# Kernel tuning notes

Measured on AMD Instinct MI355X. Metric: run time of the kernel, lower is better.

## Reference

```python
import jax, jax.numpy as jnp
import numpy as np
import math

K = 7
B, C, H, W = 16, 3, 256, 256
N = 50000
ANGLE = 30.0; TRANS = 0.45; SHEAR = 0.3; SCALE0, SCALE1 = 1.0, 0.5  # self.scale assumed [1.0,0.5] (upstream AutoDO)


def _bilinear(img, xs, ys):
    # img: (C,Hs,Ws); xs,ys: (Ho,Wo) pixel coords; border padding (clamp)
    Cc, Hs, Ws = img.shape
    xs = jnp.clip(xs, 0.0, Ws - 1.0)
    ys = jnp.clip(ys, 0.0, Hs - 1.0)
    x0 = jnp.floor(xs); y0 = jnp.floor(ys)
    wx = xs - x0; wy = ys - y0
    x0i = x0.astype(jnp.int32); y0i = y0.astype(jnp.int32)
    x1i = jnp.minimum(x0i + 1, Ws - 1); y1i = jnp.minimum(y0i + 1, Hs - 1)
    Ia = img[:, y0i, x0i]; Ib = img[:, y0i, x1i]
    Ic = img[:, y1i, x0i]; Id = img[:, y1i, x1i]
    return Ia * (1 - wx) * (1 - wy) + Ib * wx * (1 - wy) + Ic * (1 - wx) * wy + Id * wx * wy


def _resize(x, Ho, Wo):
    # torch F.interpolate bilinear, align_corners=False, no antialias
    Bb, Cc, Hs, Ws = x.shape
    ys = (jnp.arange(Ho, dtype=x.dtype) + 0.5) * (Hs / Ho) - 0.5
    xs = (jnp.arange(Wo, dtype=x.dtype) + 0.5) * (Ws / Wo) - 0.5
    Y, X = jnp.meshgrid(ys, xs, indexing='ij')
    return jax.vmap(lambda im: _bilinear(im, X, Y))(x)


def _warp_perspective(x, M, Ho, Wo):
    # kornia.warp_perspective: dst(p) = src(M^-1 p), bilinear, border padding, align_corners=True
    Bb, Cc, Hs, Ws = x.shape
    Minv = jnp.linalg.inv(M)  # (B,3,3)
    yy, xx = jnp.meshgrid(jnp.arange(Ho, dtype=x.dtype), jnp.arange(Wo, dtype=x.dtype), indexing='ij')
    pts = jnp.stack([xx.ravel(), yy.ravel(), jnp.ones(Ho * Wo, dtype=x.dtype)])  # (3, Ho*Wo)
    src = jnp.einsum('bij,jn->bin', Minv, pts)
    xs = (src[:, 0] / src[:, 2]).reshape(Bb, Ho, Wo)
    ys = (src[:, 1] / src[:, 2]).reshape(Bb, Ho, Wo)
    return jax.vmap(_bilinear)(x, xs, ys)


def _forward(x, paramP, paramM, gumbel_u, eps, idx):
    dt = x.dtype
    pP = jax.nn.sigmoid(paramP[:, idx])  # (K,B)
    logits = jnp.stack([jnp.log(pP).ravel(), jnp.log(1.0 - pP).ravel()], axis=1)  # (K*B,2)
    g = -jnp.log(-jnp.log(gumbel_u))
    y_soft = jax.nn.softmax(logits + g, axis=1)  # tau=1
    y_hard = jax.nn.one_hot(jnp.argmax(y_soft, axis=1), 2, dtype=y_soft.dtype)
    y = y_hard + y_soft - jax.lax.stop_gradient(y_soft)  # straight-through hard gumbel
    sP = y[:, 0].reshape(K, B)
    sM = jax.nn.sigmoid(paramM[:, idx]) * eps  # (K,B)
    ang = sP[0] * sM[0] * ANGLE
    # replicate torch's cat(W//2 * ones(B), H//2 * ones(B)).view(-1,2) layout exactly
    ctr = jnp.concatenate([jnp.full((B,), W // 2, dt), jnp.full((B,), H // 2, dt)]).reshape(-1, 2)
    sx = SCALE0 + sP[5] * sM[5] * SCALE1
    sy = SCALE0 + sP[6] * sM[6] * SCALE1
    rad = jnp.deg2rad(ang); ca = jnp.cos(rad); sa = jnp.sin(rad)
    # kornia get_rotation_matrix2d: rot=[[c,s],[-s,c]] @ diag(sx,sy); t = ctr - rot@ctr
    sr = jnp.stack([jnp.stack([ca * sx, sa * sy], -1), jnp.stack([-sa * sx, ca * sy], -1)], -2)  # (B,2,2)
    t = ctr - jnp.einsum('bij,bj->bi', sr, ctr)
    eye = jnp.broadcast_to(jnp.eye(3, dtype=dt), (B, 3, 3))
    R = eye.at[:, :2, :2].set(sr).at[:, :2, 2].set(t)
    T = eye.at[:, 0, 2].set(W * sP[1] * sM[1] * TRANS).at[:, 1, 2].set(H * sP[2] * sM[2] * TRANS)
    S = eye.at[:, 0, 1].set(sP[3] * sM[3] * SHEAR).at[:, 1, 0].set(sP[4] * sM[4] * SHEAR)
    M = S @ T @ R
    x_up = _resize(x, 4 * H, 4 * W)
    x_w = _warp_perspective(x_up, M, 4 * H, 4 * W)
    return _resize(x_w, H, W)


def setup_inputs() -> dict:
    key = jax.random.key(0)
    k1, k2, k3, k4 = jax.random.split(key, 4)
    p = 1.0 / (K - 2)
    prob_logit = math.log(p / (1.0 - p))
    m = 5.0 / 10.0
    magn_logit = math.log(m / (1.0 - m))
    return {
        'x': jax.random.uniform(k1, (B, C, H, W), jnp.float32),
        'paramP': jnp.full((K, N), prob_logit, jnp.float32),
        'paramM': jnp.full((K, N), magn_logit, jnp.float32),
        'gumbel_u': jax.random.uniform(k2, (K * B, 2), jnp.float32, minval=1e-6, maxval=1.0 - 1e-6),
        'eps': jax.random.normal(k3, (K, B), jnp.float32),
        'idx': jax.random.randint(k4, (B,), 0, N, jnp.int32),
    }


def reference(x, paramP, paramM, gumbel_u, eps, idx):
    return _forward(x, paramP, paramM, gumbel_u, eps, idx)
```

## Files before the change

### kernel.cpp

```cpp
#include <hip/hip_runtime.h>
#include <math.h>


typedef float floatx4 __attribute__((ext_vector_type(4)));

__device__ __forceinline__ floatx4 load4(const float* p) {
    floatx4 v;
    __builtin_memcpy(&v, p, sizeof(v));
    return v;
}

struct Up { int i0; float w; };

__device__ __forceinline__ Up upc(int v) {
    float u = fmaf(0.25f, (float)v, -0.375f);
    u = fminf(fmaxf(u, 0.0f), 255.0f);
    float f = floorf(u);
    Up r; r.i0 = (int)f; r.w = u - f;
    return r;
}

struct Trip { float w0, w1, w2; int base; };

__device__ __forceinline__ Trip merged3(float s) {
    float f = floorf(s);
    float fr = s - f;
    int v0 = (int)f;
    int v1 = min(v0 + 1, 1023);
    Up c0 = upc(v0), c1 = upc(v1);
    float A0 = 1.0f - fr, A1 = fr;
    float b0 = A1 * (1.0f - c1.w), b1 = A1 * c1.w;
    bool d = (c1.i0 != c0.i0);
    Trip t;
    t.w0 = A0 * (1.0f - c0.w) + (d ? 0.0f : b0);
    t.w1 = A0 * c0.w + (d ? b0 : b1);
    t.w2 = d ? b1 : 0.0f;
    t.base = c0.i0;
    return t;
}

__device__ __forceinline__ void pair_accum(
    Trip cA, Trip cB, Trip rA, Trip rB,
    const float* __restrict__ xb, float* acc)
{
    int cb = min(cA.base, cB.base);
    int rb = min(rA.base, rB.base);
    float CA[4], CB[4], RA[4], RB[4];
    bool sa_ = (cA.base != cb);
    CA[0] = sa_ ? 0.f : cA.w0;  CA[1] = sa_ ? cA.w0 : cA.w1;
    CA[2] = sa_ ? cA.w1 : cA.w2;  CA[3] = sa_ ? cA.w2 : 0.f;
    bool sb_ = (cB.base != cb);
    CB[0] = sb_ ? 0.f : cB.w0;  CB[1] = sb_ ? cB.w0 : cB.w1;
    CB[2] = sb_ ? cB.w1 : cB.w2;  CB[3] = sb_ ? cB.w2 : 0.f;
    bool ra_ = (rA.base != rb);
    RA[0] = ra_ ? 0.f : rA.w0;  RA[1] = ra_ ? rA.w0 : rA.w1;
    RA[2] = ra_ ? rA.w1 : rA.w2;  RA[3] = ra_ ? rA.w2 : 0.f;
    bool rb_ = (rB.base != rb);
    RB[0] = rb_ ? 0.f : rB.w0;  RB[1] = rb_ ? rB.w0 : rB.w1;
    RB[2] = rb_ ? rB.w1 : rB.w2;  RB[3] = rb_ ? rB.w2 : 0.f;

    float W[4][4];
#pragma unroll
    for (int r = 0; r < 4; ++r)
#pragma unroll
        for (int c = 0; c < 4; ++c)
            W[r][c] = fmaf(RB[r], CB[c], RA[r] * CA[c]);

    int base = cb;
    if (cb > 252) {
        int shift = cb - 252;
        base = 252;
        for (int s = 0; s < shift; ++s) {
#pragma unroll
            for (int r = 0; r < 4; ++r) {
                W[r][3] = W[r][2]; W[r][2] = W[r][1];
                W[r][1] = W[r][0]; W[r][0] = 0.f;
            }
        }
    }
    int e0 = rb * 256 + base;
    int e1 = min(rb + 1, 255) * 256 + base;
    int e2 = min(rb + 2, 255) * 256 + base;
    int e3 = min(rb + 3, 255) * 256 + base;
#pragma unroll
    for (int ch = 0; ch < 3; ++ch) {
        const float* pc = xb + ch * 65536;
        floatx4 L0 = load4(pc + e0);
        floatx4 L1 = load4(pc + e1);
        floatx4 L2 = load4(pc + e2);
        floatx4 L3 = load4(pc + e3);
        float s0 = fmaf(W[0][3], L0.w, fmaf(W[0][2], L0.z, fmaf(W[0][1], L0.y, W[0][0] * L0.x)));
        float s1 = fmaf(W[1][3], L1.w, fmaf(W[1][2], L1.z, fmaf(W[1][1], L1.y, W[1][0] * L1.x)));
        float s2 = fmaf(W[2][3], L2.w, fmaf(W[2][2], L2.z, fmaf(W[2][1], L2.y, W[2][0] * L2.x)));
        float s3 = fmaf(W[3][3], L3.w, fmaf(W[3][2], L3.z, fmaf(W[3][1], L3.y, W[3][0] * L3.x)));
        acc[ch] += (s0 + s1) + (s2 + s3);
    }
}

__global__ __launch_bounds__(256) void fused_warp(
    const float* __restrict__ x,
    const float* __restrict__ paramP, const float* __restrict__ paramM,
    const float* __restrict__ gumbel_u, const float* __restrict__ eps,
    const int* __restrict__ idx,
    float* __restrict__ out, int N)
{
    __shared__ float smem[8];

    int b = blockIdx.z;
    int tid = threadIdx.y * 16 + threadIdx.x;

    if (tid < 64) {
        float dec = 0.f, sMv = 0.f;
        if (tid < 7) {
            int k = tid;
            int id = idx[b];
            float vP = paramP[k * N + id];
            float pP = 1.0f / (1.0f + expf(-vP));
            float l0 = logf(pP);
            float l1 = logf(1.0f - pP);
            float u0 = gumbel_u[(k * 16 + b) * 2 + 0];
            float u1 = gumbel_u[(k * 16 + b) * 2 + 1];
            float g0 = -logf(-logf(u0));
            float g1 = -logf(-logf(u1));
            dec = (l0 + g0 >= l1 + g1) ? 1.0f : 0.0f;
            float vM = paramM[k * N + id];
            float sig = 1.0f / (1.0f + expf(-vM));
            sMv = sig * eps[k * 16 + b];
        }
        float sP[7], sM[7];
#pragma unroll
        for (int k = 0; k < 7; ++k) {
            sP[k] = __shfl(dec, k, 64);
            sM[k] = __shfl(sMv, k, 64);
        }
        if (tid == 0) {
            float ang = sP[0] * sM[0] * 30.0f;
            float rad = ang * 0.017453292519943295f;
            float ca = cosf(rad), sa = sinf(rad);
            float sx = 1.0f + sP[5] * sM[5] * 0.5f;
            float sy = 1.0f + sP[6] * sM[6] * 0.5f;
            float sr00 = ca * sx, sr01 = sa * sy;
            float sr10 = -sa * sx, sr11 = ca * sy;
            float t0 = 128.0f - (sr00 + sr01) * 128.0f;
            float t1 = 128.0f - (sr10 + sr11) * 128.0f;
            float tx2 = 256.0f * sP[1] * sM[1] * 0.45f;
            float ty2 = 256.0f * sP[2] * sM[2] * 0.45f;
            float sh01 = sP[3] * sM[3] * 0.3f;
            float sh10 = sP[4] * sM[4] * 0.3f;
            float e0 = t0 + tx2, e1 = t1 + ty2;
            float a  = sr00 + sh01 * sr10;
            float bb = sr01 + sh01 * sr11;
            float txm = e0 + sh01 * e1;
            float c  = sh10 * sr00 + sr10;
            float d  = sh10 * sr01 + sr11;
            float tym = sh10 * e0 + e1;
            float det = a * d - bb * c;
            float rdet = 1.0f / det;
            smem[0] = d * rdet;
            smem[1] = -bb * rdet;
            smem[2] = (bb * tym - d * txm) * rdet;
            smem[3] = -c * rdet;
            smem[4] = a * rdet;
            smem[5] = (c * txm - a * tym) * rdet;
        }
    }
    __syncthreads();

    float m00 = smem[0], m01 = smem[1], m02 = smem[2];
    float m10 = smem[3], m11 = smem[4], m12 = smem[5];

    int wid  = tid >> 6;
    int lane = tid & 63;
    int lx = lane & 7, ly = lane >> 3;
    int j = blockIdx.x * 16 + ((wid & 1) * 8 + lx);
    int i = blockIdx.y * 16 + ((wid >> 1) * 8 + ly);

    const float* xb = x + b * 3 * 65536;

    float XA = (float)(4 * j + 1);
    float Y0 = (float)(4 * i + 1);
    float x0 = fmaf(m00, XA, fmaf(m01, Y0, m02));
    float y0 = fmaf(m10, XA, fmaf(m11, Y0, m12));
    float xs[4], ys[4];
    xs[0] = x0;        ys[0] = y0;
    xs[1] = x0 + m00;  ys[1] = y0 + m10;
    xs[2] = x0 + m01;  ys[2] = y0 + m11;
    xs[3] = xs[1] + m01; ys[3] = ys[1] + m11;

    Trip cx[4], ry[4];
#pragma unroll
    for (int s = 0; s < 4; ++s) {
        cx[s] = merged3(fminf(fmaxf(xs[s], 0.f), 1023.f));
        ry[s] = merged3(fminf(fmaxf(ys[s], 0.f), 1023.f));
    }

    int cbmin = min(min(cx[0].base, cx[1].base), min(cx[2].base, cx[3].base));
    int cbmax = max(max(cx[0].base, cx[1].base), max(cx[2].base, cx[3].base));
    int rbmin = min(min(ry[0].base, ry[1].base), min(ry[2].base, ry[3].base));
    int rbmax = max(max(ry[0].base, ry[1].base), max(ry[2].base, ry[3].base));

    float acc[3] = {0.f, 0.f, 0.f};

    if (((cbmax - cbmin) | (rbmax - rbmin)) <= 1) {
        float W[4][4];
#pragma unroll
        for (int s = 0; s < 4; ++s) {
            bool sc = (cx[s].base != cbmin);
            float C0 = sc ? 0.f : cx[s].w0;
            float C1 = sc ? cx[s].w0 : cx[s].w1;
            float C2 = sc ? cx[s].w1 : cx[s].w2;
            float C3 = sc ? cx[s].w2 : 0.f;
            bool sr = (ry[s].base != rbmin);
            float R0 = sr ? 0.f : ry[s].w0;
            float R1 = sr ? ry[s].w0 : ry[s].w1;
            float R2 = sr ? ry[s].w1 : ry[s].w2;
            float R3 = sr ? ry[s].w2 : 0.f;
            float C[4] = {C0, C1, C2, C3};
            float R[4] = {R0, R1, R2, R3};
            if (s == 0) {
#pragma unroll
                for (int r = 0; r < 4; ++r)
#pragma unroll
                    for (int c = 0; c < 4; ++c)
                        W[r][c] = R[r] * C[c];
            } else {
#pragma unroll
                for (int r = 0; r < 4; ++r)
#pragma unroll
                    for (int c = 0; c < 4; ++c)
                        W[r][c] = fmaf(R[r], C[c], W[r][c]);
            }
        }

        int base = cbmin;
        if (cbmin > 252) {
            int shift = cbmin - 252;
            base = 252;
            for (int s = 0; s < shift; ++s) {
#pragma unroll
                for (int r = 0; r < 4; ++r) {
                    W[r][3] = W[r][2]; W[r][2] = W[r][1];
                    W[r][1] = W[r][0]; W[r][0] = 0.f;
                }
            }
        }

        int e0 = rbmin * 256 + base;
        int e1 = min(rbmin + 1, 255) * 256 + base;
        int e2 = min(rbmin + 2, 255) * 256 + base;
        int e3 = min(rbmin + 3, 255) * 256 + base;
#pragma unroll
        for (int ch = 0; ch < 3; ++ch) {
            const float* pc = xb + ch * 65536;
            floatx4 L0 = load4(pc + e0);
            floatx4 L1 = load4(pc + e1);
            floatx4 L2 = load4(pc + e2);
            floatx4 L3 = load4(pc + e3);
            float s0 = fmaf(W[0][3], L0.w, fmaf(W[0][2], L0.z, fmaf(W[0][1], L0.y, W[0][0] * L0.x)));
            float s1 = fmaf(W[1][3], L1.w, fmaf(W[1][2], L1.z, fmaf(W[1][1], L1.y, W[1][0] * L1.x)));
            float s2 = fmaf(W[2][3], L2.w, fmaf(W[2][2], L2.z, fmaf(W[2][1], L2.y, W[2][0] * L2.x)));
            float s3 = fmaf(W[3][3], L3.w, fmaf(W[3][2], L3.z, fmaf(W[3][1], L3.y, W[3][0] * L3.x)));
            acc[ch] = (s0 + s1) + (s2 + s3);
        }
    } else {
        pair_accum(cx[0], cx[1], ry[0], ry[1], xb, acc);
        pair_accum(cx[2], cx[3], ry[2], ry[3], xb, acc);
    }

    int obase = ((b * 3) * 256 + i) * 256 + j;
    out[obase]          = 0.25f * acc[0];
    out[obase + 65536]  = 0.25f * acc[1];
    out[obase + 131072] = 0.25f * acc[2];
}

extern "C" void kernel_launch(void* const* d_in, const int* in_sizes, int n_in,
                              void* d_out, int out_size, void* d_ws, size_t ws_size,
                              hipStream_t stream) {
    const float* x      = (const float*)d_in[0];
    const float* paramP = (const float*)d_in[1];
    const float* paramM = (const float*)d_in[2];
    const float* gumbel = (const float*)d_in[3];
    const float* eps    = (const float*)d_in[4];
    const int*   idx    = (const int*)d_in[5];
    float* out = (float*)d_out;
    int N = in_sizes[1] / 7;

    hipLaunchKernelGGL(fused_warp, dim3(16, 16, 16), dim3(16, 16, 1), 0, stream,
                       x, paramP, paramM, gumbel, eps, idx, out, N);
}
```

Before: 87.74 us.

## Stage per-block source footprint in LDS for the fast gather path

Each block computes the bounding box of its warped source footprint and, when the box fits in 40x40, cooperatively loads that tile for all three channels into shared memory. The fast 4x4 weighted-gather path then reads from LDS instead of issuing unaligned global vector loads per thread. Blocks whose footprint is too large, and the pair_accum path, keep reading global memory. The cost is an extra barrier, about 19KB of shared memory per block that may lower occupancy, scalar LDS reads that can bank-conflict, and more branching.

```diff
diff --git a/kernel.cpp b/kernel.cpp
--- a/kernel.cpp
+++ b/kernel.cpp
@@ -3,6 +3,11 @@
 
 
 typedef float floatx4 __attribute__((ext_vector_type(4)));
+typedef float floatx2 __attribute__((ext_vector_type(2)));
+
+#define SH 40
+#define SW 40
+#define PLANE (SH * SW)
 
 __device__ __forceinline__ floatx4 load4(const float* p) {
     floatx4 v;
@@ -105,6 +110,7 @@
     float* __restrict__ out, int N)
 {
     __shared__ float smem[8];
+    __shared__ float lds[3 * PLANE];
 
     int b = blockIdx.z;
     int tid = threadIdx.y * 16 + threadIdx.x;
@@ -169,13 +175,60 @@
     float m00 = smem[0], m01 = smem[1], m02 = smem[2];
     float m10 = smem[3], m11 = smem[4], m12 = smem[5];
 
+    const float* xb = x + b * 3 * 65536;
+
+    float X0 = (float)(4 * (blockIdx.x * 16) + 1), X1 = X0 + 61.0f;
+    float Yc0 = (float)(4 * (blockIdx.y * 16) + 1), Yc1 = Yc0 + 61.0f;
+    float xmin = 1e30f, xmax = -1e30f, ymin = 1e30f, ymax = -1e30f;
+#pragma unroll
+    for (int cxk = 0; cxk < 2; ++cxk)
+#pragma unroll
+        for (int cyk = 0; cyk < 2; ++cyk) {
+            float Xc = cxk ? X1 : X0;
+            float Yk = cyk ? Yc1 : Yc0;
+            float xsv = fmaf(m00, Xc, fmaf(m01, Yk, m02));
+            float ysv = fmaf(m10, Xc, fmaf(m11, Yk, m12));
+            xmin = fminf(xmin, xsv); xmax = fmaxf(xmax, xsv);
+            ymin = fminf(ymin, ysv); ymax = fmaxf(ymax, ysv);
+        }
+    xmin = fminf(fmaxf(xmin, 0.f), 1023.f);
+    xmax = fminf(fmaxf(xmax, 0.f), 1023.f);
+    ymin = fminf(fmaxf(ymin, 0.f), 1023.f);
+    ymax = fminf(fmaxf(ymax, 0.f), 1023.f);
+    int cmin = min(max((int)floorf(fmaf(0.25f, xmin, -0.375f)) - 1, 0), 255);
+    int cmax = min(max((int)floorf(fmaf(0.25f, xmax, -0.375f)) + 4, 0), 255);
+    int rmin = min(max((int)floorf(fmaf(0.25f, ymin, -0.375f)) - 1, 0), 255);
+    int rmax = min(max((int)floorf(fmaf(0.25f, ymax, -0.375f)) + 4, 0), 255);
+    cmin &= ~1;
+    bool fits = (cmax - cmin + 1 <= SW) && (rmax - rmin + 1 <= SH);
+
+    if (fits) {
+#pragma unroll
+        for (int ch = 0; ch < 3; ++ch) {
+            const float* pc = xb + ch * 65536;
+            float* lp = lds + ch * PLANE;
+#pragma unroll
+            for (int it = 0; it < 4; ++it) {
+                int pidx = it * 256 + tid;
+                if (pidx < 800) {
+                    int r  = pidx / 20;
+                    int c2 = pidx - r * 20;
+                    int row = min(rmin + r, 255);
+                    int col = min(cmin + c2 * 2, 254);
+                    floatx2 v;
+                    __builtin_memcpy(&v, pc + row * 256 + col, sizeof(v));
+                    *(floatx2*)(lp + r * SW + c2 * 2) = v;
+                }
+            }
+        }
+    }
+    __syncthreads();
+
     int wid  = tid >> 6;
     int lane = tid & 63;
     int lx = lane & 7, ly = lane >> 3;
     int j = blockIdx.x * 16 + ((wid & 1) * 8 + lx);
     int i = blockIdx.y * 16 + ((wid >> 1) * 8 + ly);
-
-    const float* xb = x + b * 3 * 65536;
 
     float XA = (float)(4 * j + 1);
     float Y0 = (float)(4 * i + 1);
@@ -232,35 +285,52 @@
             }
         }
 
-        int base = cbmin;
-        if (cbmin > 252) {
-            int shift = cbmin - 252;
-            base = 252;
-            for (int s = 0; s < shift; ++s) {
-#pragma unroll
-                for (int r = 0; r < 4; ++r) {
-                    W[r][3] = W[r][2]; W[r][2] = W[r][1];
-                    W[r][1] = W[r][0]; W[r][0] = 0.f;
+        if (fits) {
+            int cl[4], ro[4];
+#pragma unroll
+            for (int k = 0; k < 4; ++k) {
+                cl[k] = min(min(cbmin + k, 255), cmax) - cmin;
+                ro[k] = (min(min(rbmin + k, 255), rmax) - rmin) * SW;
+            }
+#pragma unroll
+            for (int ch = 0; ch < 3; ++ch) {
+                const float* lc = lds + ch * PLANE;
+                float s0 = fmaf(W[0][3], lc[ro[0] + cl[3]], fmaf(W[0][2], lc[ro[0] + cl[2]], fmaf(W[0][1], lc[ro[0] + cl[1]], W[0][0] * lc[ro[0] + cl[0]])));
+                float s1 = fmaf(W[1][3], lc[ro[1] + cl[3]], fmaf(W[1][2], lc[ro[1] + cl[2]], fmaf(W[1][1], lc[ro[1] + cl[1]], W[1][0] * lc[ro[1] + cl[0]])));
+                float s2 = fmaf(W[2][3], lc[ro[2] + cl[3]], fmaf(W[2][2], lc[ro[2] + cl[2]], fmaf(W[2][1], lc[ro[2] + cl[1]], W[2][0] * lc[ro[2] + cl[0]])));
+                float s3 = fmaf(W[3][3], lc[ro[3] + cl[3]], fmaf(W[3][2], lc[ro[3] + cl[2]], fmaf(W[3][1], lc[ro[3] + cl[1]], W[3][0] * lc[ro[3] + cl[0]])));
+                acc[ch] = (s0 + s1) + (s2 + s3);
+            }
+        } else {
+            int base = cbmin;
+            if (cbmin > 252) {
+                int shift = cbmin - 252;
+                base = 252;
+                for (int s = 0; s < shift; ++s) {
+#pragma unroll
+                    for (int r = 0; r < 4; ++r) {
+                        W[r][3] = W[r][2]; W[r][2] = W[r][1];
+                        W[r][1] = W[r][0]; W[r][0] = 0.f;
+                    }
                 }
             }
-        }
-
-        int e0 = rbmin * 256 + base;
-        int e1 = min(rbmin + 1, 255) * 256 + base;
-        int e2 = min(rbmin + 2, 255) * 256 + base;
-        int e3 = min(rbmin + 3, 255) * 256 + base;
-#pragma unroll
-        for (int ch = 0; ch < 3; ++ch) {
-            const float* pc = xb + ch * 65536;
-            floatx4 L0 = load4(pc + e0);
-            floatx4 L1 = load4(pc + e1);
-            floatx4 L2 = load4(pc + e2);
-            floatx4 L3 = load4(pc + e3);
-            float s0 = fmaf(W[0][3], L0.w, fmaf(W[0][2], L0.z, fmaf(W[0][1], L0.y, W[0][0] * L0.x)));
-            float s1 = fmaf(W[1][3], L1.w, fmaf(W[1][2], L1.z, fmaf(W[1][1], L1.y, W[1][0] * L1.x)));
-            float s2 = fmaf(W[2][3], L2.w, fmaf(W[2][2], L2.z, fmaf(W[2][1], L2.y, W[2][0] * L2.x)));
-            float s3 = fmaf(W[3][3], L3.w, fmaf(W[3][2], L3.z, fmaf(W[3][1], L3.y, W[3][0] * L3.x)));
-            acc[ch] = (s0 + s1) + (s2 + s3);
+            int e0 = rbmin * 256 + base;
+            int e1 = min(rbmin + 1, 255) * 256 + base;
+            int e2 = min(rbmin + 2, 255) * 256 + base;
+            int e3 = min(rbmin + 3, 255) * 256 + base;
+#pragma unroll
+            for (int ch = 0; ch < 3; ++ch) {
+                const float* pc = xb + ch * 65536;
+                floatx4 L0 = load4(pc + e0);
+                floatx4 L1 = load4(pc + e1);
+                floatx4 L2 = load4(pc + e2);
+                floatx4 L3 = load4(pc + e3);
+                float s0 = fmaf(W[0][3], L0.w, fmaf(W[0][2], L0.z, fmaf(W[0][1], L0.y, W[0][0] * L0.x)));
+                float s1 = fmaf(W[1][3], L1.w, fmaf(W[1][2], L1.z, fmaf(W[1][1], L1.y, W[1][0] * L1.x)));
+                float s2 = fmaf(W[2][3], L2.w, fmaf(W[2][2], L2.z, fmaf(W[2][1], L2.y, W[2][0] * L2.x)));
+                float s3 = fmaf(W[3][3], L3.w, fmaf(W[3][2], L3.z, fmaf(W[3][1], L3.y, W[3][0] * L3.x)));
+                acc[ch] = (s0 + s1) + (s2 + s3);
+            }
         }
     } else {
         pair_accum(cx[0], cx[1], ry[0], ry[1], xb, acc);
```

After: 102.2 us. 16.5% more time.
